# Optimization experiments

Measured on AMD Instinct MI355X. Metric: run time of the kernel, lower is better.

## Reference

```python
import jax, jax.numpy as jnp
import numpy as np

TWO_PI = 2.0 * np.pi


def _fftfreq(n, d):
    # numpy-compatible fftfreq, trace/grad-safe in d: [0..n/2-1, -n/2..-1]/(n*d)
    k = jnp.arange(n)
    k = jnp.where(k < (n + 1) // 2, k, k - n).astype(jnp.float32)
    return k / (n * d)


def _forward(x, wp1_re, wp1_im, wp2_re, wp2_im, wr_re, wr_im, ty, tx):
    wp1 = (wp1_re + 1j * wp1_im).astype(jnp.complex64)   # [Ci,Co,m1]
    wp2 = (wp2_re + 1j * wp2_im).astype(jnp.complex64)   # [Ci,Co,m2]
    wr = (wr_re + 1j * wr_im).astype(jnp.complex64)      # [Ci,Co,m1,m2]
    Ny, Nx = x.shape[-2], x.shape[-1]
    dty = ty[1] - ty[0]
    dtx = tx[1] - tx[0]

    alpha = jnp.fft.fft2(x, axes=(-2, -1))               # [B,Ci,Ny,Nx] complex
    lam1 = (1j * TWO_PI * _fftfreq(Ny, dty)).astype(jnp.complex64)  # [Ny]
    lam2 = (1j * TWO_PI * _fftfreq(Nx, dtx)).astype(jnp.complex64)  # [Nx]

    # Pole-residue transfer function factors: Hw = wr / ((lam1-p1)(lam2-p2))
    A1 = 1.0 / (lam1 - wp1[..., None])                   # [Ci,Co,m1,Ny]
    A2 = 1.0 / (lam2 - wp2[..., None])                   # [Ci,Co,m2,Nx]

    # sum over poles (p,q) of Hw -> [Ci,Co,Ny,Nx]
    Hsum = jnp.einsum('ikpq,ikpo,ikqx->ikox', wr, A1, A2)
    res1 = jnp.einsum('biox,ikox->bkox', alpha, Hsum)    # [B,Co,Ny,Nx]
    # sum over frequency grid (o,x) -> residue coefficients [B,Co,m1,m2]
    res2 = jnp.einsum('biox,ikpq,ikpo,ikqx->bkpq', alpha, wr, A1, A2)

    x1 = jnp.real(jnp.fft.ifft2(res1, s=(Ny, Nx), axes=(-2, -1)))

    # explicit pole-exponential evaluation over the spatial grid
    E1 = jnp.exp(wp1[..., None] * ty.astype(jnp.complex64))  # [Ci,Co,m1,Ny]
    E2 = jnp.exp(wp2[..., None] * tx.astype(jnp.complex64))  # [Ci,Co,m2,Nx]
    # res2 channel dim contracts against E1/E2's first (in==out required)
    x2 = jnp.real(jnp.einsum('kbpq,bipz,biqx->kizx', res2, E1, E2)) / (Nx * Ny)
    return x1 + x2


def setup_inputs() -> dict:
    key = jax.random.key(0)
    B, Ci, Co, Ny, Nx, m1, m2 = 8, 32, 32, 128, 128, 4, 5
    ks = jax.random.split(key, 7)
    scale = 1.0 / (Ci * Co)
    x = jax.random.normal(ks[0], (B, Ci, Ny, Nx), jnp.float32)
    wp1_re = scale * jax.random.uniform(ks[1], (Ci, Co, m1), jnp.float32)
    wp1_im = scale * jax.random.uniform(ks[2], (Ci, Co, m1), jnp.float32)
    wp2_re = scale * jax.random.uniform(ks[3], (Ci, Co, m2), jnp.float32)
    wp2_im = scale * jax.random.uniform(ks[4], (Ci, Co, m2), jnp.float32)
    wr_re = scale * jax.random.uniform(ks[5], (Ci, Co, m1, m2), jnp.float32)
    wr_im = scale * jax.random.uniform(ks[6], (Ci, Co, m1, m2), jnp.float32)
    ty = (jnp.arange(Ny) / Ny).astype(jnp.float32)
    tx = (jnp.arange(Nx) / Nx).astype(jnp.float32)
    return dict(x=x, wp1_re=wp1_re, wp1_im=wp1_im, wp2_re=wp2_re, wp2_im=wp2_im,
                wr_re=wr_re, wr_im=wr_im, ty=ty, tx=tx)


def reference(x, wp1_re, wp1_im, wp2_re, wp2_im, wr_re, wr_im, ty, tx):
    return _forward(x, wp1_re, wp1_im, wp2_re, wp2_im, wr_re, wr_im, ty, tx)
```

## Files before the change

### kernel.cpp

```cpp
#include <hip/hip_runtime.h>
#include <math.h>

#define N 128
#define B 8
#define CI 32
#define CO 32
#define M1 4
#define M2 5
#define IK (CI*CO)
#define IKP (IK*M1)
#define IKQ (IK*M2)
#define TWO_PI_F 6.2831853071795864769f

__device__ __forceinline__ float2 cmul(float2 a, float2 b){
    return make_float2(fmaf(a.x,b.x,-(a.y*b.y)), fmaf(a.x,b.y,a.y*b.x));
}
__device__ __forceinline__ float2 cmadd(float2 acc, float2 a, float2 b){
    acc.x = fmaf(a.x, b.x, fmaf(-a.y, b.y, acc.x));
    acc.y = fmaf(a.x, b.y, fmaf( a.y, b.x, acc.y));
    return acc;
}

__global__ void k_A1T(const float* wr_, const float* wi_, const float* t_, float2* A1T){
    int idx = blockIdx.x*256 + threadIdx.x;
    int o   = idx >> 12;
    int ikp = idx & (IKP-1);
    float d = t_[1]-t_[0];
    float invnd = 1.0f/((float)N*d);
    int kk = (o < N/2) ? o : o - N;
    float lam = TWO_PI_F * (float)kk * invnd;
    float dr = -wr_[ikp];
    float di = lam - wi_[ikp];
    float inv = 1.0f/(dr*dr + di*di);
    A1T[idx] = make_float2(dr*inv, -di*inv);
}

__global__ void k_A2(const float* wr_, const float* wi_, const float* t_, float2* A2){
    int idx = blockIdx.x*256 + threadIdx.x;
    int ikq = idx >> 7; int xx = idx & (N-1);
    float d = t_[1]-t_[0];
    float invnd = 1.0f/((float)N*d);
    int kk = (xx < N/2) ? xx : xx - N;
    float lam = TWO_PI_F * (float)kk * invnd;
    float dr = -wr_[ikq];
    float di = lam - wi_[ikq];
    float inv = 1.0f/(dr*dr + di*di);
    A2[idx] = make_float2(dr*inv, -di*inv);
}

__global__ void k_E(const float* wr_, const float* wi_, const float* t_, float2* E){
    int idx = blockIdx.x*256 + threadIdx.x;
    int ikp = idx >> 7; int y = idx & (N-1);
    float t = t_[y];
    float m = expf(wr_[ikp]*t);
    float s, c; sincosf(wi_[ikp]*t, &s, &c);
    E[idx] = make_float2(m*c, m*s);
}

__global__ void k_W2N(const float* wrr, const float* wri, const float2* A2, float2* W2N){
    int idx = blockIdx.x*256 + threadIdx.x;
    int ikp = idx >> 7; int xx = idx & (N-1);
    int ik = ikp >> 2; int p = ikp & 3;
    float2 acc = make_float2(0.f,0.f);
    const float* wr0 = wrr + ik*(M1*M2) + p*M2;
    const float* wi0 = wri + ik*(M1*M2) + p*M2;
    const float2* a2 = A2 + (size_t)ik*(M2*N) + xx;
    #pragma unroll
    for(int q=0;q<M2;q++){
        float2 w = make_float2(wr0[q], wi0[q]);
        acc = cmadd(acc, w, a2[q*N]);
    }
    W2N[(size_t)ikp*N + xx] = acc;
}

template<int SIGNPOS, int REALIN, int SCALE>
__global__ void __launch_bounds__(256) k_fft_rows(const void* in_, float2* out){
    const float sgn = SIGNPOS ? 1.0f : -1.0f;
    __shared__ float tre[16*132];
    __shared__ float tim_[16*132];
    __shared__ float zre[16*136];
    __shared__ float zim[16*136];
    int t = threadIdx.x;
    size_t row0 = (size_t)blockIdx.x * 16;

    if(REALIN){
        const float* src = (const float*)in_ + row0*N;
        #pragma unroll
        for(int j=0;j<8;j++){
            int idx = t + 256*j; int r = idx>>7, cl = idx&127;
            tre[r*132+cl] = src[idx];
        }
    } else {
        const float2* src = (const float2*)in_ + row0*N;
        #pragma unroll
        for(int j=0;j<8;j++){
            int idx = t + 256*j; int r = idx>>7, cl = idx&127;
            float2 v = src[idx];
            tre[r*132+cl] = v.x; tim_[r*132+cl] = v.y;
        }
    }
    float t16c[16], t16s[16];
    #pragma unroll
    for(int j=0;j<16;j++){ float s,c; sincosf(sgn*(TWO_PI_F/16.f)*(float)j, &s,&c); t16c[j]=c; t16s[j]=s; }
    __syncthreads();

    int r = t>>4, u = t&15, b = u&7, h = u>>3;
    float xr[16], xi[16];
    #pragma unroll
    for(int a=0;a<16;a++){
        float vr = tre[r*132 + 8*a + b];
        float vi = REALIN ? 0.f : tim_[r*132 + 8*a + b];
        if(h && (a&1)){ vr = -vr; vi = -vi; }
        xr[a]=vr; xi[a]=vi;
    }
    #pragma unroll
    for(int cc=0; cc<8; cc++){
        float yr=0.f, yi=0.f;
        #pragma unroll
        for(int a=0;a<16;a++){
            int j = (a*cc)&15;
            if(REALIN){
                yr = fmaf(xr[a], t16c[j], yr);
                yi = fmaf(xr[a], t16s[j], yi);
            } else {
                yr = fmaf(xr[a], t16c[j], yr); yr = fmaf(-xi[a], t16s[j], yr);
                yi = fmaf(xr[a], t16s[j], yi); yi = fmaf( xi[a], t16c[j], yi);
            }
        }
        int c = 8*h + cc;
        float s,co; sincosf(sgn*(TWO_PI_F/128.f)*(float)(b*c), &s,&co);
        zre[r*136 + b*17 + c] = fmaf(yr,co,-(yi*s));
        zim[r*136 + b*17 + c] = fmaf(yr,s,  yi*co);
    }
    __syncthreads();

    float t8c[8], t8s[8];
    #pragma unroll
    for(int j=0;j<8;j++){ float s,c; sincosf(sgn*(TWO_PI_F/8.f)*(float)j, &s,&c); t8c[j]=c; t8s[j]=s; }
    int r2 = t>>4, c2 = t&15;
    float zr_[8], zi_[8];
    #pragma unroll
    for(int bb=0;bb<8;bb++){ zr_[bb]=zre[r2*136 + bb*17 + c2]; zi_[bb]=zim[r2*136 + bb*17 + c2]; }
    float2* dst = out + (row0 + r2)*N;
    #pragma unroll
    for(int d=0; d<8; d++){
        float Xr=0.f, Xi=0.f;
        #pragma unroll
        for(int bb=0;bb<8;bb++){
            int j=(bb*d)&7;
            Xr = fmaf(zr_[bb], t8c[j], Xr); Xr = fmaf(-zi_[bb], t8s[j], Xr);
            Xi = fmaf(zr_[bb], t8s[j], Xi); Xi = fmaf( zi_[bb], t8c[j], Xi);
        }
        if(SCALE){ Xr *= (1.f/128.f); Xi *= (1.f/128.f); }
        dst[c2 + 16*d] = make_float2(Xr, Xi);
    }
}

template<int SIGNPOS, int REALOUT, int SCALE>
__global__ void __launch_bounds__(256) k_fft_cols(const float2* in, float2* outc, float* outr){
    const float sgn = SIGNPOS ? 1.0f : -1.0f;
    __shared__ float tre[N*17];
    __shared__ float tim_[N*17];
    __shared__ float zre[8*16*17];
    __shared__ float zim[8*16*17];
    int t = threadIdx.x;
    int img = blockIdx.x >> 3; int x0 = (blockIdx.x & 7)*16;
    const float2* src = in + (size_t)img*N*N + x0;
    #pragma unroll
    for(int j=0;j<8;j++){
        int idx = t + 256*j; int y = idx>>4, xc = idx&15;
        float2 v = src[y*N + xc];
        tre[y*17+xc]=v.x; tim_[y*17+xc]=v.y;
    }
    float t16c[16], t16s[16];
    #pragma unroll
    for(int j=0;j<16;j++){ float s,c; sincosf(sgn*(TWO_PI_F/16.f)*(float)j, &s,&c); t16c[j]=c; t16s[j]=s; }
    __syncthreads();

    int xc = t&15, u = t>>4, b = u&7, h = u>>3;
    float xr[16], xi[16];
    #pragma unroll
    for(int a=0;a<16;a++){
        int y = 8*a + b;
        float vr = tre[y*17+xc];
        float vi = tim_[y*17+xc];
        if(h && (a&1)){ vr = -vr; vi = -vi; }
        xr[a]=vr; xi[a]=vi;
    }
    #pragma unroll
    for(int cc=0; cc<8; cc++){
        float yr=0.f, yi=0.f;
        #pragma unroll
        for(int a=0;a<16;a++){
            int j = (a*cc)&15;
            yr = fmaf(xr[a], t16c[j], yr); yr = fmaf(-xi[a], t16s[j], yr);
            yi = fmaf(xr[a], t16s[j], yi); yi = fmaf( xi[a], t16c[j], yi);
        }
        int c = 8*h + cc;
        float s,co; sincosf(sgn*(TWO_PI_F/128.f)*(float)(b*c), &s,&co);
        zre[(b*16 + c)*17 + xc] = fmaf(yr,co,-(yi*s));
        zim[(b*16 + c)*17 + xc] = fmaf(yr,s,  yi*co);
    }
    __syncthreads();

    float t8c[8], t8s[8];
    #pragma unroll
    for(int j=0;j<8;j++){ float s,c; sincosf(sgn*(TWO_PI_F/8.f)*(float)j, &s,&c); t8c[j]=c; t8s[j]=s; }
    int c2 = t>>4; int x2 = t&15;
    float zr_[8], zi_[8];
    #pragma unroll
    for(int bb=0;bb<8;bb++){ zr_[bb]=zre[(bb*16 + c2)*17 + x2]; zi_[bb]=zim[(bb*16 + c2)*17 + x2]; }
    #pragma unroll
    for(int d=0; d<8; d++){
        float Xr=0.f, Xi=0.f;
        #pragma unroll
        for(int bb=0;bb<8;bb++){
            int j=(bb*d)&7;
            Xr = fmaf(zr_[bb], t8c[j], Xr); Xr = fmaf(-zi_[bb], t8s[j], Xr);
            Xi = fmaf(zr_[bb], t8s[j], Xi); Xi = fmaf( zi_[bb], t8c[j], Xi);
        }
        int ky = c2 + 16*d;
        if(REALOUT){
            outr[(size_t)img*N*N + ky*N + x0 + x2] = Xr * (SCALE ? (1.f/128.f) : 1.f);
        } else {
            if(SCALE){ Xr *= (1.f/128.f); Xi *= (1.f/128.f); }
            outc[(size_t)img*N*N + ky*N + x0 + x2] = make_float2(Xr, Xi);
        }
    }
}

__global__ void __launch_bounds__(256) k_res1(const float2* alpha, const float2* A1T,
                                              const float2* W2N, float2* res1){
    __shared__ float4 At4[B*CI*8];
    int t = threadIdx.x;
    int o  = blockIdx.x >> 3;
    int x0 = (blockIdx.x & 7) * 16;

    {
        int im0 = t >> 3, xq = t & 7;
        #pragma unroll
        for(int j=0;j<8;j++){
            int im = im0 + 32*j;
            At4[im*8 + xq] = *(const float4*)(alpha + (size_t)im*(N*N) + o*N + x0 + 2*xq);
        }
    }
    __syncthreads();

    int k = t >> 3, xh = t & 7;
    float2 acc[B][2];
    #pragma unroll
    for(int b=0;b<B;b++){ acc[b][0]=make_float2(0.f,0.f); acc[b][1]=make_float2(0.f,0.f); }

    const float2* a1base = A1T + (size_t)o*IKP + k*M1;
    const float2* w2base = W2N + ((size_t)k*M1)*N + x0 + 2*xh;

    #pragma unroll 2
    for(int i=0;i<CI;i++){
        float4 a1a = *(const float4*)(a1base + (size_t)i*128);
        float4 a1b = *(const float4*)(a1base + (size_t)i*128 + 2);
        float2 a1v[M1] = { make_float2(a1a.x,a1a.y), make_float2(a1a.z,a1a.w),
                           make_float2(a1b.x,a1b.y), make_float2(a1b.z,a1b.w) };
        float2 h0 = make_float2(0.f,0.f), h1 = make_float2(0.f,0.f);
        const float2* w2 = w2base + (size_t)i*(128*N);
        #pragma unroll
        for(int p=0;p<M1;p++){
            float4 wv = *(const float4*)(w2 + (size_t)p*N);
            h0 = cmadd(h0, a1v[p], make_float2(wv.x,wv.y));
            h1 = cmadd(h1, a1v[p], make_float2(wv.z,wv.w));
        }
        #pragma unroll
        for(int b=0;b<B;b++){
            float4 av = At4[(b*CI + i)*8 + xh];
            acc[b][0] = cmadd(acc[b][0], make_float2(av.x,av.y), h0);
            acc[b][1] = cmadd(acc[b][1], make_float2(av.z,av.w), h1);
        }
    }

    #pragma unroll
    for(int b=0;b<B;b++){
        float4 v = make_float4(acc[b][0].x, acc[b][0].y, acc[b][1].x, acc[b][1].y);
        *(float4*)(res1 + (size_t)(b*CO + k)*(N*N) + o*N + x0 + 2*xh) = v;
    }
}

__global__ void __launch_bounds__(256) k_S_res2(const float2* alpha, const float2* A2,
                                                const float2* A1T, const float* wrr,
                                                const float* wri, float2* res2){
    __shared__ float2 tile[128*17];
    __shared__ float2 A2c[16*40];
    int t = threadIdx.x;
    int ol = t & 31;
    int kl = t >> 5;
    int bid = blockIdx.x;
    int kq = bid & 3;
    int i  = (bid >> 2) & (CI-1);
    int b  = bid >> 7;
    int k0 = kq*8;
    int k  = k0 + kl;
    int ik = i*CO + k;
    const float2* asrc = alpha + ((size_t)(b*CI + i))*(N*N);

    const int trow = t >> 4, txc = t & 15;
    int a2dst[3]; size_t a2src[3]; bool a2ok[3];
    #pragma unroll
    for(int s=0;s<3;s++){
        int e = t + 256*s;
        a2ok[s] = (e < 640);
        int e2 = a2ok[s] ? e : 0;
        int xcs = e2 / 40, rs = e2 - xcs*40;
        int kk = rs / 5, qq = rs - kk*5;
        a2dst[s] = xcs*40 + rs;
        a2src[s] = ((size_t)(i*CO + k0 + kk)*M2 + qq)*N + xcs;
    }

    float2 U[4][5];
    #pragma unroll
    for(int oi=0;oi<4;oi++)
        #pragma unroll
        for(int q=0;q<5;q++) U[oi][q] = make_float2(0.f,0.f);

    float2 pre[8], a2pre[3];
    #pragma unroll
    for(int j=0;j<8;j++) pre[j] = asrc[(trow + 16*j)*N + txc];
    #pragma unroll
    for(int s=0;s<3;s++) if(a2ok[s]) a2pre[s] = A2[a2src[s]];

    for(int c=0; c<8; c++){
        __syncthreads();
        #pragma unroll
        for(int j=0;j<8;j++) tile[(trow + 16*j)*17 + txc] = pre[j];
        #pragma unroll
        for(int s=0;s<3;s++) if(a2ok[s]) A2c[a2dst[s]] = a2pre[s];
        if(c < 7){
            int x0n = (c+1)*16;
            #pragma unroll
            for(int j=0;j<8;j++) pre[j] = asrc[(trow + 16*j)*N + x0n + txc];
            #pragma unroll
            for(int s=0;s<3;s++) if(a2ok[s]) a2pre[s] = A2[a2src[s] + x0n];
        }
        __syncthreads();
        #pragma unroll 4
        for(int xc=0; xc<16; xc++){
            float2 a2v[5];
            const float2* a2row = A2c + xc*40 + kl*5;
            #pragma unroll
            for(int q=0;q<5;q++) a2v[q] = a2row[q];
            #pragma unroll
            for(int oi=0;oi<4;oi++){
                float2 av = tile[(ol + 32*oi)*17 + xc];
                #pragma unroll
                for(int q=0;q<5;q++) U[oi][q] = cmadd(U[oi][q], av, a2v[q]);
            }
        }
    }

    float2 S[4][5];
    #pragma unroll
    for(int p=0;p<4;p++)
        #pragma unroll
        for(int q=0;q<5;q++) S[p][q] = make_float2(0.f,0.f);
    #pragma unroll
    for(int oi=0;oi<4;oi++){
        int o = ol + 32*oi;
        const float2* a1 = A1T + (size_t)o*IKP + (size_t)ik*M1;
        float2 a1v[4];
        #pragma unroll
        for(int p=0;p<4;p++) a1v[p] = a1[p];
        #pragma unroll
        for(int p=0;p<4;p++)
            #pragma unroll
            for(int q=0;q<5;q++) S[p][q] = cmadd(S[p][q], a1v[p], U[oi][q]);
    }
    #pragma unroll
    for(int m=1;m<32;m<<=1){
        #pragma unroll
        for(int p=0;p<4;p++)
            #pragma unroll
            for(int q=0;q<5;q++){
                S[p][q].x += __shfl_xor(S[p][q].x, m);
                S[p][q].y += __shfl_xor(S[p][q].y, m);
            }
    }
    if(ol==0){
        const float* wr0 = wrr + ik*(M1*M2);
        const float* wi0 = wri + ik*(M1*M2);
        float2* dst = res2 + (size_t)(b*CO + k)*(M1*M2);
        #pragma unroll
        for(int p=0;p<4;p++)
            #pragma unroll
            for(int q=0;q<5;q++){
                float2 w = make_float2(wr0[p*5+q], wi0[p*5+q]);
                float2 v = cmul(w, S[p][q]);
                atomicAdd(&dst[p*5+q].x, v.x);
                atomicAdd(&dst[p*5+q].y, v.y);
            }
    }
}

__global__ void __launch_bounds__(256) k_x2(const float2* res2, const float2* E1,
                                            const float2* E2, float* out){
    __shared__ float2 Wt[M1][N];
    __shared__ float2 E1s[M1][N];
    int t = threadIdx.x;
    int ys = blockIdx.x & 3;
    int j = (blockIdx.x >> 2) & 31;
    int b = blockIdx.x >> 7;
    int xx = t & (N-1); int hb = t >> 7;
    float acc[16];
    #pragma unroll
    for(int r=0;r<16;r++) acc[r]=0.f;
    for(int c=0;c<CI;c++){
        int ikcj = c*CO + j;
        __syncthreads();
        #pragma unroll
        for(int s=0;s<2;s++){
            int e = t + 256*s;
            int pp = e >> 7; int xi = e & (N-1);
            float2 w = make_float2(0.f,0.f);
            const float2* r2 = res2 + (size_t)(b*CO + c)*(M1*M2) + pp*M2;
            const float2* e2 = E2 + ((size_t)ikcj*M2)*N + xi;
            #pragma unroll
            for(int q=0;q<M2;q++) w = cmadd(w, r2[q], e2[q*N]);
            Wt[pp][xi] = w;
            E1s[pp][xi] = E1[((size_t)ikcj*M1 + pp)*N + xi];
        }
        __syncthreads();
        float2 wreg[M1];
        #pragma unroll
        for(int p=0;p<M1;p++) wreg[p] = Wt[p][xx];
        #pragma unroll
        for(int r=0;r<16;r++){
            int y = 8*r + 2*ys + hb;
            float s = acc[r];
            #pragma unroll
            for(int p=0;p<M1;p++){
                float2 e = E1s[p][y];
                s = fmaf(e.x, wreg[p].x, s); s = fmaf(-e.y, wreg[p].y, s);
            }
            acc[r] = s;
        }
    }
    const float sc = 1.0f/((float)N*(float)N);
    size_t base = (size_t)(b*CO + j)*(N*N);
    #pragma unroll
    for(int r=0;r<16;r++){
        size_t idx = base + (size_t)(8*r + 2*ys + hb)*N + xx;
        out[idx] += acc[r]*sc;
    }
}

extern "C" void kernel_launch(void* const* d_in, const int* in_sizes, int n_in,
                              void* d_out, int out_size, void* d_ws, size_t ws_size,
                              hipStream_t stream){
    const float* x    = (const float*)d_in[0];
    const float* wp1r = (const float*)d_in[1];
    const float* wp1i = (const float*)d_in[2];
    const float* wp2r = (const float*)d_in[3];
    const float* wp2i = (const float*)d_in[4];
    const float* wrr  = (const float*)d_in[5];
    const float* wri  = (const float*)d_in[6];
    const float* ty   = (const float*)d_in[7];
    const float* tx   = (const float*)d_in[8];
    float* out = (float*)d_out;
    float2* ws = (float2*)d_ws;

    const size_t NCIMG = (size_t)B*CI*N*N;
    float2* bufA  = ws;
    float2* alpha = bufA  + NCIMG;
    float2* res1  = alpha + NCIMG;
    float2* A1T   = res1  + NCIMG;
    float2* A2    = A1T   + (size_t)N*IKP;
    float2* W2N   = A2    + (size_t)IKQ*N;
    float2* E1    = W2N   + (size_t)N*IKP;
    float2* E2    = E1    + (size_t)IKP*N;
    float2* res2  = E2    + (size_t)IKQ*N;

    k_A1T<<<(N*IKP)/256, 256, 0, stream>>>(wp1r, wp1i, ty, A1T);
    k_E  <<<(IKP*N)/256, 256, 0, stream>>>(wp1r, wp1i, ty, E1);
    k_A2 <<<(IKQ*N)/256, 256, 0, stream>>>(wp2r, wp2i, tx, A2);
    k_E  <<<(IKQ*N)/256, 256, 0, stream>>>(wp2r, wp2i, tx, E2);
    k_W2N<<<(IKP*N)/256, 256, 0, stream>>>(wrr, wri, A2, W2N);

    k_fft_rows<0,1,0><<<(B*CI*N)/16, 256, 0, stream>>>((const void*)x, bufA);
    k_fft_cols<0,0,0><<<B*CI*8, 256, 0, stream>>>(bufA, alpha, nullptr);

    hipMemsetAsync(res2, 0, (size_t)B*CO*M1*M2*sizeof(float2), stream);
    k_res1<<<N*8, 256, 0, stream>>>(alpha, A1T, W2N, res1);
    k_S_res2<<<B*CI*4, 256, 0, stream>>>(alpha, A2, A1T, wrr, wri, res2);

    k_fft_rows<1,0,1><<<(B*CO*N)/16, 256, 0, stream>>>((const void*)res1, bufA);
    k_fft_cols<1,1,1><<<B*CO*8, 256, 0, stream>>>(bufA, nullptr, out);
    k_x2<<<B*CO*4, 256, 0, stream>>>(res2, E1, E2, out);
}
```

Measured before the change: 364.6 us.

## Retile k_x2 with register blocking, staged res2, and double-buffered E1/E2 prefetch

```diff
diff --git a/kernel.cpp b/kernel.cpp
--- a/kernel.cpp
+++ b/kernel.cpp
@@ -399,53 +399,109 @@
 
 __global__ void __launch_bounds__(256) k_x2(const float2* res2, const float2* E1,
                                             const float2* E2, float* out){
-    __shared__ float2 Wt[M1][N];
-    __shared__ float2 E1s[M1][N];
+    __shared__ __align__(16) float2 res2s[CI*M1*M2];
+    __shared__ __align__(16) float2 Wt[M1*N];
+    __shared__ __align__(16) float2 buf[2][M1*64 + M2*N];
     int t = threadIdx.x;
-    int ys = blockIdx.x & 3;
-    int j = (blockIdx.x >> 2) & 31;
-    int b = blockIdx.x >> 7;
-    int xx = t & (N-1); int hb = t >> 7;
-    float acc[16];
-    #pragma unroll
-    for(int r=0;r<16;r++) acc[r]=0.f;
-    for(int c=0;c<CI;c++){
-        int ikcj = c*CO + j;
-        __syncthreads();
+    int yh = blockIdx.x & 1;
+    int j  = (blockIdx.x >> 1) & (CO-1);
+    int b  = blockIdx.x >> 6;
+    int xt = t & 15, yt = t >> 4;
+
+    {
+        const float4* s4 = (const float4*)(res2 + (size_t)b*CO*M1*M2);
+        float4* d4 = (float4*)res2s;
+        d4[t] = s4[t];
+        if(t < 64) d4[256+t] = s4[256+t];
+    }
+
+    const bool is1_0 = (t < 128);
+    const bool ok1 = (t < 192);
+    int off0, dst0;
+    if(is1_0){ int pp = t >> 5, rem = t & 31; off0 = pp*N + rem*2; dst0 = pp*64 + rem*2; }
+    else     { int g = t - 128; int qq = g >> 6, xi = (g & 63) << 1; off0 = qq*N + xi; dst0 = 256 + qq*128 + xi; }
+    int qq1 = 2 + (t >> 6), xi1 = (t & 63) << 1;
+    int off1 = qq1*N + xi1;
+    int dst1 = 256 + qq1*128 + xi1;
+
+    const float2* E1c = E1 + ((size_t)j*M1)*N + yh*64;
+    const float2* E2c = E2 + ((size_t)j*M2)*N;
+
+    float4 pre0 = *(const float4*)((is1_0 ? E1c : E2c) + off0);
+    float4 pre1 = ok1 ? *(const float4*)(E2c + off1) : make_float4(0.f,0.f,0.f,0.f);
+    *(float4*)(&buf[0][dst0]) = pre0;
+    if(ok1) *(float4*)(&buf[0][dst1]) = pre1;
+    int cur = 0;
+    __syncthreads();
+
+    float acc[4][8];
+    #pragma unroll
+    for(int yy=0;yy<4;yy++)
+        #pragma unroll
+        for(int s=0;s<8;s++) acc[yy][s] = 0.f;
+
+    for(int c=0; c<CI; c++){
+        const float2* E2s = buf[cur] + 256;
         #pragma unroll
         for(int s=0;s<2;s++){
             int e = t + 256*s;
-            int pp = e >> 7; int xi = e & (N-1);
+            int pp = e >> 7, xi = e & 127;
+            const float2* rr = res2s + c*(M1*M2) + pp*M2;
             float2 w = make_float2(0.f,0.f);
-            const float2* r2 = res2 + (size_t)(b*CO + c)*(M1*M2) + pp*M2;
-            const float2* e2 = E2 + ((size_t)ikcj*M2)*N + xi;
-            #pragma unroll
-            for(int q=0;q<M2;q++) w = cmadd(w, r2[q], e2[q*N]);
-            Wt[pp][xi] = w;
-            E1s[pp][xi] = E1[((size_t)ikcj*M1 + pp)*N + xi];
+            #pragma unroll
+            for(int q=0;q<M2;q++) w = cmadd(w, rr[q], E2s[q*128 + xi]);
+            Wt[pp*128 + xi] = w;
+        }
+        if(c+1 < CI){
+            E1c += (size_t)CO*M1*N;
+            E2c += (size_t)CO*M2*N;
+            pre0 = *(const float4*)((is1_0 ? E1c : E2c) + off0);
+            if(ok1) pre1 = *(const float4*)(E2c + off1);
         }
         __syncthreads();
-        float2 wreg[M1];
-        #pragma unroll
-        for(int p=0;p<M1;p++) wreg[p] = Wt[p][xx];
-        #pragma unroll
-        for(int r=0;r<16;r++){
-            int y = 8*r + 2*ys + hb;
-            float s = acc[r];
-            #pragma unroll
-            for(int p=0;p<M1;p++){
-                float2 e = E1s[p][y];
-                s = fmaf(e.x, wreg[p].x, s); s = fmaf(-e.y, wreg[p].y, s);
+
+        const float2* E1s = buf[cur];
+        float2 e1[4][4];
+        #pragma unroll
+        for(int p=0;p<4;p++){
+            float4 a  = *(const float4*)(E1s + p*64 + yt*4);
+            float4 bq = *(const float4*)(E1s + p*64 + yt*4 + 2);
+            e1[p][0]=make_float2(a.x,a.y);  e1[p][1]=make_float2(a.z,a.w);
+            e1[p][2]=make_float2(bq.x,bq.y); e1[p][3]=make_float2(bq.z,bq.w);
+        }
+        #pragma unroll
+        for(int p=0;p<4;p++){
+            #pragma unroll
+            for(int s=0;s<4;s++){
+                float4 wv = *(const float4*)(Wt + p*128 + 32*s + 2*xt);
+                #pragma unroll
+                for(int yy=0;yy<4;yy++){
+                    float2 e = e1[p][yy];
+                    acc[yy][2*s]   = fmaf(e.x, wv.x, fmaf(-e.y, wv.y, acc[yy][2*s]));
+                    acc[yy][2*s+1] = fmaf(e.x, wv.z, fmaf(-e.y, wv.w, acc[yy][2*s+1]));
+                }
             }
-            acc[r] = s;
-        }
-    }
+        }
+        if(c+1 < CI){
+            float2* nb = buf[cur^1];
+            *(float4*)(nb + dst0) = pre0;
+            if(ok1) *(float4*)(nb + dst1) = pre1;
+        }
+        cur ^= 1;
+        __syncthreads();
+    }
+
     const float sc = 1.0f/((float)N*(float)N);
-    size_t base = (size_t)(b*CO + j)*(N*N);
-    #pragma unroll
-    for(int r=0;r<16;r++){
-        size_t idx = base + (size_t)(8*r + 2*ys + hb)*N + xx;
-        out[idx] += acc[r]*sc;
+    size_t base = (size_t)(b*CO + j)*(N*N) + (size_t)yh*64*N;
+    #pragma unroll
+    for(int yy=0;yy<4;yy++){
+        float* orow = out + base + (size_t)(yt*4 + yy)*N;
+        #pragma unroll
+        for(int s=0;s<4;s++){
+            float2* dst = (float2*)(orow + 32*s + 2*xt);
+            float2 old = *dst;
+            *dst = make_float2(old.x + acc[yy][2*s]*sc, old.y + acc[yy][2*s+1]*sc);
+        }
     }
 }
 
@@ -490,5 +546,5 @@
 
     k_fft_rows<1,0,1><<<(B*CO*N)/16, 256, 0, stream>>>((const void*)res1, bufA);
     k_fft_cols<1,1,1><<<B*CO*8, 256, 0, stream>>>(bufA, nullptr, out);
-    k_x2<<<B*CO*4, 256, 0, stream>>>(res2, E1, E2, out);
-}
+    k_x2<<<B*CO*2, 256, 0, stream>>>(res2, E1, E2, out);
+}
```

Result: faster. 355.2 us (-2.6%).
